# Performance work log

Measured on AMD Instinct MI355X. Metric: run time of the kernel, lower is better.

## Reference

```python
import jax, jax.numpy as jnp
import numpy as np

TAU = 2.0      # LIF membrane time constant (spikingjelly default-style, decay_input=True)
VTH = 0.5      # v_threshold from init
S = 4          # time_steps
EPS = 1e-5     # BatchNorm eps
ALPHA = 4.0    # surrogate sigmoid alpha (spikingjelly Sigmoid default)

@jax.custom_vjp
def spike(x):
    # Heaviside forward (spikingjelly: x >= 0 -> 1)
    return (x >= 0.0).astype(x.dtype)

def _spike_fwd(x):
    return spike(x), x

def _spike_bwd(x, g):
    sg = jax.nn.sigmoid(ALPHA * x)
    return (g * ALPHA * sg * (1.0 - sg),)

spike.defvjp(_spike_fwd, _spike_bwd)

def bn(y, gamma, beta, mean, var):
    # inference-mode BatchNorm2d over channel axis 1; y: (B, C, T, V)
    inv = gamma * jax.lax.rsqrt(var + EPS)
    return y * inv[None, :, None, None] + (beta - mean * inv)[None, :, None, None]


def setup_inputs() -> dict:
    key = jax.random.key(0)
    ks = jax.random.split(key, 16)
    B, T, C, V, H, NC = 16, 512, 3, 16, 128, 12
    inp = {
        "x": jax.random.normal(ks[0], (B, T, C, V), dtype=jnp.float32),
        "w1": jax.random.normal(ks[1], (H, C), dtype=jnp.float32) * (1.0 / np.sqrt(C)),
        "b1": jax.random.normal(ks[2], (H,), dtype=jnp.float32) * 0.01,
        "g1": jnp.ones((H,), jnp.float32),
        "be1": jnp.zeros((H,), jnp.float32),
        "m1": jax.random.normal(ks[3], (H,), dtype=jnp.float32) * 0.1,
        "rv1": jax.random.uniform(ks[4], (H,), dtype=jnp.float32) + 0.5,
        "w2": jax.random.normal(ks[5], (H, H), dtype=jnp.float32) * (1.0 / np.sqrt(H)),
        "b2": jax.random.normal(ks[6], (H,), dtype=jnp.float32) * 0.01,
        "g2": jnp.ones((H,), jnp.float32),
        "be2": jnp.zeros((H,), jnp.float32),
        "m2": jax.random.normal(ks[7], (H,), dtype=jnp.float32) * 0.1,
        "rv2": jax.random.uniform(ks[8], (H,), dtype=jnp.float32) + 0.5,
        "wc": jax.random.normal(ks[9], (NC, H), dtype=jnp.float32) * (1.0 / np.sqrt(H)),
        "bc": jax.random.normal(ks[10], (NC,), dtype=jnp.float32) * 0.01,
    }
    return inp


def reference(x, w1, b1, g1, be1, m1, rv1, w2, b2, g2, be2, m2, rv2, wc, bc):
    # x: (B, T, C, V) -> channels-first (B, C, T, V) as in torch permute
    xc = jnp.transpose(x, (0, 2, 1, 3))
    # fc1 1x1 conv + BN; input identical across all S steps, so compute once
    h1 = bn(jnp.einsum('bctv,oc->botv', xc, w1) + b1[None, :, None, None],
            g1, be1, m1, rv1)  # (B, H, T, V)

    def step(carry, _):
        v1s, v2s, acc = carry
        # LIF1: decay_input=True, v_reset=0 hard reset
        v1n = v1s + (h1 - v1s) / TAU
        s1 = spike(v1n - VTH)
        v1n = v1n * (1.0 - s1)
        # fc2 1x1 conv + BN on spikes
        h2 = bn(jnp.einsum('botv,po->bptv', s1, w2) + b2[None, :, None, None],
                g2, be2, m2, rv2)
        # LIF2
        v2n = v2s + (h2 - v2s) / TAU
        s2 = spike(v2n - VTH)
        v2n = v2n * (1.0 - s2)
        return (v1n, v2n, acc + s2), None

    z = jnp.zeros_like(h1)
    (_, _, acc), _ = jax.lax.scan(step, (z, z, z), None, length=S)
    # mean over S, then mean over T and V -> (B, H); dropout is identity in eval
    feat = (acc / S).mean(axis=(2, 3))
    return feat @ wc.T + bc
```

## Files before the change

### kernel.cpp

```cpp
#include <hip/hip_runtime.h>
#include <hip/hip_bf16.h>
#include <stdint.h>
#include <math.h>

#define B_ 16
#define T_ 512
#define V_ 16
#define H_ 128
#define NC_ 12

typedef float v2f __attribute__((ext_vector_type(2)));
typedef __attribute__((ext_vector_type(8))) short s8frag;
typedef __attribute__((ext_vector_type(16))) float f16frag;
typedef unsigned long long u64;


__device__ __forceinline__ unsigned short bf16_rne(float w) {
    unsigned u = __float_as_uint(w);
    unsigned r = (u + 0x7FFFu + ((u >> 16) & 1u)) >> 16;
    return (unsigned short)r;
}
__device__ __forceinline__ float bf16_f32(unsigned short h) {
    return __uint_as_float((unsigned)h << 16);
}
__device__ __forceinline__ void split8(const float* __restrict__ s, s8frag& hi, s8frag& lo) {
    #pragma unroll
    for (int j = 0; j < 8; ++j) {
        float w = s[j];
        unsigned short hb = bf16_rne(w);
        unsigned short lb = bf16_rne(w - bf16_f32(hb));
        hi[j] = (short)hb;
        lo[j] = (short)lb;
    }
}
__device__ __forceinline__ uint4 expand8(unsigned bt) {
    uint4 r;
    r.x = ((bt      & 1u) * 0x3F80u) | (((bt >> 1) & 1u) * 0x3F800000u);
    r.y = (((bt >> 2) & 1u) * 0x3F80u) | (((bt >> 3) & 1u) * 0x3F800000u);
    r.z = (((bt >> 4) & 1u) * 0x3F80u) | (((bt >> 5) & 1u) * 0x3F800000u);
    r.w = (((bt >> 6) & 1u) * 0x3F80u) | (((bt >> 7) & 1u) * 0x3F800000u);
    return r;
}

#define ROUNDS 8
__global__ __launch_bounds__(256, 3) void snn_main(
    const float* __restrict__ x,
    const float* __restrict__ w1, const float* __restrict__ b1,
    const float* __restrict__ g1, const float* __restrict__ be1,
    const float* __restrict__ m1, const float* __restrict__ rv1,
    const float* __restrict__ w2, const float* __restrict__ b2,
    const float* __restrict__ g2, const float* __restrict__ be2,
    const float* __restrict__ m2, const float* __restrict__ rv2,
    float* __restrict__ feat)
{
    __shared__ uint4 afrag[2][2][8][64];
    __shared__ uint4 msk[4][16];

    const int tid  = threadIdx.x;
    const int lane = tid & 63;
    const int wv   = tid >> 6;
    const int nl   = lane & 15;
    const int kg   = (lane >> 4) & 1;
    const int ch4  = lane >> 5;
    const int bb   = blockIdx.x >> 6;
    const int sbase = (blockIdx.x & 63) * (ROUNDS * 16);

    const int p = lane, q = lane + 64;
    v2f w0v = { w1[p*3+0], w1[q*3+0] };
    v2f w1v = { w1[p*3+1], w1[q*3+1] };
    v2f w2v = { w1[p*3+2], w1[q*3+2] };
    v2f b1v = { b1[p], b1[q] };
    float i1a = g1[p] * (float)(1.0 / sqrt((double)(rv1[p] + 1e-5f)));
    float i1b = g1[q] * (float)(1.0 / sqrt((double)(rv1[q] + 1e-5f)));
    v2f i1v = { i1a, i1b };
    v2f d1v = { be1[p] - m1[p] * i1a, be1[q] - m1[q] * i1b };

    const int chn = wv * 32 + (lane & 31);
    float i2c = g2[chn] * (float)(1.0 / sqrt((double)(rv2[chn] + 1e-5f)));
    float d2c = be2[chn] - m2[chn] * i2c;
    float b2c = b2[chn];

    s8frag bh[8], bl[8];
    #pragma unroll
    for (int c = 0; c < 8; ++c)
        split8(&w2[chn * H_ + c * 16 + ch4 * 8], bh[c], bl[c]);

    float facc = 0.f;

    #define CONSUME(BUF)                                                        \
        for (int tt = 0; tt < 2; ++tt) {                                        \
            f16frag acch = {0.f,0.f,0.f,0.f,0.f,0.f,0.f,0.f,                    \
                            0.f,0.f,0.f,0.f,0.f,0.f,0.f,0.f};                   \
            f16frag accl = acch;                                                \
            _Pragma("unroll")                                                   \
            for (int c = 0; c < 8; ++c) {                                       \
                s8frag a = *(const s8frag*)&afrag[BUF][tt][c][lane];            \
                acch = __builtin_amdgcn_mfma_f32_32x32x16_bf16(a, bh[c], acch, 0,0,0); \
                accl = __builtin_amdgcn_mfma_f32_32x32x16_bf16(a, bl[c], accl, 0,0,0); \
            }                                                                   \
            f16frag accs = acch + accl;                                         \
            _Pragma("unroll")                                                   \
            for (int g = 0; g < 4; ++g) {                                       \
                float v = 0.f;                                                  \
                _Pragma("unroll")                                               \
                for (int s = 0; s < 4; ++s) {                                   \
                    float h2 = (accs[g*4+s] + b2c) * i2c + d2c;                 \
                    v = v + (h2 - v) * 0.5f;                                    \
                    bool sp = v >= 0.5f;                                        \
                    v = sp ? 0.f : v;                                           \
                    facc += sp ? 1.f : 0.f;                                     \
                }                                                               \
            }                                                                   \
        }

    for (int r = 0; r < ROUNDS; ++r) {
        #pragma unroll
        for (int i = 0; i < 4; ++i) {
            int site = sbase + r * 16 + wv * 4 + i;
            int t = site >> 4, v = site & 15;
            const float* xp = x + ((size_t)(bb * T_ + t) * 3) * V_ + v;
            float x0 = xp[0], x1 = xp[V_], x2 = xp[2 * V_];

            v2f h1 = ((x0 * w0v + x1 * w1v + x2 * w2v) + b1v) * i1v + d1v;
            v2f v1t = h1 * 0.5f;
            v2f v2t = v1t + h1 * 0.25f;
            v2f v3t = v2t + (h1 - v2t) * 0.5f;
            v2f v4t = v3t + (h1 - v3t) * 0.5f;

            u64 t1a = __ballot(v1t.x >= 0.5f), t2a = __ballot(v2t.x >= 0.5f);
            u64 t3a = __ballot(v3t.x >= 0.5f), t4a = __ballot(v4t.x >= 0.5f);
            u64 t1b = __ballot(v1t.y >= 0.5f), t2b = __ballot(v2t.y >= 0.5f);
            u64 t3b = __ballot(v3t.y >= 0.5f), t4b = __ballot(v4t.y >= 0.5f);
            u64 s3a = t1a | (t3a & ~t2a), s3b = t1b | (t3b & ~t2b);
            u64 s4a = t2a | (t4a & ~t3a), s4b = t2b | (t4b & ~t3b);

            u64 mx = (lane == 0) ? t1a : (lane == 1) ? t2a : (lane == 2) ? s3a : s4a;
            u64 my = (lane == 0) ? t1b : (lane == 1) ? t2b : (lane == 2) ? s3b : s4b;
            if (lane < 4) {
                uint4 mm;
                mm.x = (unsigned)mx; mm.y = (unsigned)(mx >> 32);
                mm.z = (unsigned)my; mm.w = (unsigned)(my >> 32);
                msk[wv][i * 4 + lane] = mm;
            }
        }
        {
            uint4 mm = msk[wv][nl];
            u64 wsel = ch4 ? ((u64)mm.z | ((u64)mm.w << 32))
                           : ((u64)mm.x | ((u64)mm.y << 32));
            int tt   = wv >> 1;
            int slot = ((wv & 1) * 16 + nl) + 32 * kg;
            int buf  = r & 1;
            #pragma unroll
            for (int j = 0; j < 4; ++j) {
                unsigned by = (unsigned)(wsel >> (kg * 8 + j * 16)) & 0xFFu;
                afrag[buf][tt][ch4 * 4 + j][slot] = expand8(by);
            }
        }
        if (r > 0) { int pb = (r - 1) & 1; CONSUME(pb); }
        __syncthreads();
    }
    { int pb = (ROUNDS - 1) & 1; CONSUME(pb); }
    #undef CONSUME

    facc += __shfl_xor(facc, 32);
    if (lane < 32) atomicAdd(&feat[bb * H_ + chn], facc);
}

__global__ __launch_bounds__(128) void classifier_kernel(
    const float* __restrict__ feat,
    const float* __restrict__ wc,
    const float* __restrict__ bc,
    float* __restrict__ out) {
    __shared__ float fb[H_];
    int b = blockIdx.x, t = threadIdx.x;
    fb[t] = feat[b * H_ + t] * (1.0f / 32768.0f);
    __syncthreads();
    if (t < NC_) {
        float s = 0.f;
        for (int h = 0; h < H_; ++h) s += fb[h] * wc[t * H_ + h];
        out[b * NC_ + t] = s + bc[t];
    }
}

extern "C" void kernel_launch(void* const* d_in, const int* in_sizes, int n_in,
                              void* d_out, int out_size, void* d_ws, size_t ws_size,
                              hipStream_t stream) {
    const float* x   = (const float*)d_in[0];
    const float* w1  = (const float*)d_in[1];
    const float* b1  = (const float*)d_in[2];
    const float* g1  = (const float*)d_in[3];
    const float* be1 = (const float*)d_in[4];
    const float* m1  = (const float*)d_in[5];
    const float* rv1 = (const float*)d_in[6];
    const float* w2  = (const float*)d_in[7];
    const float* b2  = (const float*)d_in[8];
    const float* g2  = (const float*)d_in[9];
    const float* be2 = (const float*)d_in[10];
    const float* m2  = (const float*)d_in[11];
    const float* rv2 = (const float*)d_in[12];
    const float* wc  = (const float*)d_in[13];
    const float* bc  = (const float*)d_in[14];

    float* feat = (float*)d_ws;
    float* out  = (float*)d_out;

    snn_main<<<1024, 256, 0, stream>>>(x, w1, b1, g1, be1, m1, rv1,
                                       w2, b2, g2, be2, m2, rv2, feat);
    classifier_kernel<<<B_, 128, 0, stream>>>(feat, wc, bc, out);
}
```

Before: 141.5 us.

## Fuse classifier into main kernel, fold BN into weights, expand spikes in registers

Several changes land together. The BN2 scale is folded into the split bf16 weights and the bias is folded into the accumulator init. Spike masks are stored as u64 words in shared memory and expanded to bf16 fragments in registers inside the MFMA loop, replacing the pre-expanded afrag buffer. The grid doubles to 2048 blocks of 4 rounds with launch bounds relaxed, and a last-block-done atomic counter computes the classifier in the same kernel, removing the second launch. The done counter is never reset between calls and feat is still not zeroed in the kernel, so the code relies on the harness clearing the workspace; otherwise repeated calls break the last-block test.

```diff
diff --git a/kernel.cpp b/kernel.cpp
--- a/kernel.cpp
+++ b/kernel.cpp
@@ -23,10 +23,11 @@
 __device__ __forceinline__ float bf16_f32(unsigned short h) {
     return __uint_as_float((unsigned)h << 16);
 }
-__device__ __forceinline__ void split8(const float* __restrict__ s, s8frag& hi, s8frag& lo) {
+__device__ __forceinline__ void split8s(const float* __restrict__ s, float scale,
+                                        s8frag& hi, s8frag& lo) {
     #pragma unroll
     for (int j = 0; j < 8; ++j) {
-        float w = s[j];
+        float w = s[j] * scale;
         unsigned short hb = bf16_rne(w);
         unsigned short lb = bf16_rne(w - bf16_f32(hb));
         hi[j] = (short)hb;
@@ -42,8 +43,8 @@
     return r;
 }
 
-#define ROUNDS 8
-__global__ __launch_bounds__(256, 3) void snn_main(
+#define ROUNDS 4
+__global__ __launch_bounds__(256) void snn_main(
     const float* __restrict__ x,
     const float* __restrict__ w1, const float* __restrict__ b1,
     const float* __restrict__ g1, const float* __restrict__ be1,
@@ -51,19 +52,24 @@
     const float* __restrict__ w2, const float* __restrict__ b2,
     const float* __restrict__ g2, const float* __restrict__ be2,
     const float* __restrict__ m2, const float* __restrict__ rv2,
-    float* __restrict__ feat)
+    const float* __restrict__ wc, const float* __restrict__ bc,
+    float* __restrict__ feat, float* __restrict__ done,
+    float* __restrict__ out)
 {
-    __shared__ uint4 afrag[2][2][8][64];
-    __shared__ uint4 msk[4][16];
+    __shared__ union {
+        u64   msk[2][128];
+        float fb[B_ * H_];
+    } sh;
+    __shared__ float lastf;
 
     const int tid  = threadIdx.x;
     const int lane = tid & 63;
     const int wv   = tid >> 6;
-    const int nl   = lane & 15;
-    const int kg   = (lane >> 4) & 1;
-    const int ch4  = lane >> 5;
-    const int bb   = blockIdx.x >> 6;
-    const int sbase = (blockIdx.x & 63) * (ROUNDS * 16);
+    const int hl5  = lane >> 5;
+    const int si   = (lane & 31) >> 2;
+    const int st   = lane & 3;
+    const int bb   = blockIdx.x >> 7;
+    const int sbase = (blockIdx.x & 127) * (ROUNDS * 16);
 
     const int p = lane, q = lane + 64;
     v2f w0v = { w1[p*3+0], w1[q*3+0] };
@@ -78,23 +84,31 @@
     const int chn = wv * 32 + (lane & 31);
     float i2c = g2[chn] * (float)(1.0 / sqrt((double)(rv2[chn] + 1e-5f)));
     float d2c = be2[chn] - m2[chn] * i2c;
-    float b2c = b2[chn];
+    float e2  = b2[chn] * i2c + d2c;
 
     s8frag bh[8], bl[8];
     #pragma unroll
     for (int c = 0; c < 8; ++c)
-        split8(&w2[chn * H_ + c * 16 + ch4 * 8], bh[c], bl[c]);
+        split8s(&w2[chn * H_ + c * 16 + hl5 * 8], i2c, bh[c], bl[c]);
 
     float facc = 0.f;
 
-    #define CONSUME(BUF)                                                        \
+    #define CONSUME(PB)                                                         \
+        _Pragma("unroll")                                                       \
         for (int tt = 0; tt < 2; ++tt) {                                        \
-            f16frag acch = {0.f,0.f,0.f,0.f,0.f,0.f,0.f,0.f,                    \
-                            0.f,0.f,0.f,0.f,0.f,0.f,0.f,0.f};                   \
-            f16frag accl = acch;                                                \
+            u64 mm0 = sh.msk[PB][(tt * 8 + si) * 8 + st * 2 + 0];               \
+            u64 mm1 = sh.msk[PB][(tt * 8 + si) * 8 + st * 2 + 1];               \
+            f16frag acch = { e2,e2,e2,e2,e2,e2,e2,e2,                           \
+                             e2,e2,e2,e2,e2,e2,e2,e2 };                         \
+            f16frag accl = { 0.f,0.f,0.f,0.f,0.f,0.f,0.f,0.f,                   \
+                             0.f,0.f,0.f,0.f,0.f,0.f,0.f,0.f };                 \
             _Pragma("unroll")                                                   \
             for (int c = 0; c < 8; ++c) {                                       \
-                s8frag a = *(const s8frag*)&afrag[BUF][tt][c][lane];            \
+                u64 src = (c < 4) ? mm0 : mm1;                                  \
+                unsigned by = (unsigned)(src >> (((c & 3) * 2 + hl5) * 8)) & 0xFFu; \
+                uint4 fr = expand8(by);                                         \
+                s8frag a;                                                       \
+                ((uint4*)&a)[0] = fr;                                           \
                 acch = __builtin_amdgcn_mfma_f32_32x32x16_bf16(a, bh[c], acch, 0,0,0); \
                 accl = __builtin_amdgcn_mfma_f32_32x32x16_bf16(a, bl[c], accl, 0,0,0); \
             }                                                                   \
@@ -104,7 +118,7 @@
                 float v = 0.f;                                                  \
                 _Pragma("unroll")                                               \
                 for (int s = 0; s < 4; ++s) {                                   \
-                    float h2 = (accs[g*4+s] + b2c) * i2c + d2c;                 \
+                    float h2 = accs[g * 4 + s];                                 \
                     v = v + (h2 - v) * 0.5f;                                    \
                     bool sp = v >= 0.5f;                                        \
                     v = sp ? 0.f : v;                                           \
@@ -116,7 +130,8 @@
     for (int r = 0; r < ROUNDS; ++r) {
         #pragma unroll
         for (int i = 0; i < 4; ++i) {
-            int site = sbase + r * 16 + wv * 4 + i;
+            int sl   = wv * 4 + i;
+            int site = sbase + r * 16 + sl;
             int t = site >> 4, v = site & 15;
             const float* xp = x + ((size_t)(bb * T_ + t) * 3) * V_ + v;
             float x0 = xp[0], x1 = xp[V_], x2 = xp[2 * V_];
@@ -134,51 +149,35 @@
             u64 s3a = t1a | (t3a & ~t2a), s3b = t1b | (t3b & ~t2b);
             u64 s4a = t2a | (t4a & ~t3a), s4b = t2b | (t4b & ~t3b);
 
-            u64 mx = (lane == 0) ? t1a : (lane == 1) ? t2a : (lane == 2) ? s3a : s4a;
-            u64 my = (lane == 0) ? t1b : (lane == 1) ? t2b : (lane == 2) ? s3b : s4b;
-            if (lane < 4) {
-                uint4 mm;
-                mm.x = (unsigned)mx; mm.y = (unsigned)(mx >> 32);
-                mm.z = (unsigned)my; mm.w = (unsigned)(my >> 32);
-                msk[wv][i * 4 + lane] = mm;
+            u64 mA = (lane == 0) ? t1a : (lane == 2) ? t2a : (lane == 4) ? s3a : s4a;
+            u64 mB = (lane == 1) ? t1b : (lane == 3) ? t2b : (lane == 5) ? s3b : s4b;
+            if (lane < 8) {
+                sh.msk[r & 1][sl * 8 + lane] = (lane & 1) ? mB : mA;
             }
         }
-        {
-            uint4 mm = msk[wv][nl];
-            u64 wsel = ch4 ? ((u64)mm.z | ((u64)mm.w << 32))
-                           : ((u64)mm.x | ((u64)mm.y << 32));
-            int tt   = wv >> 1;
-            int slot = ((wv & 1) * 16 + nl) + 32 * kg;
-            int buf  = r & 1;
-            #pragma unroll
-            for (int j = 0; j < 4; ++j) {
-                unsigned by = (unsigned)(wsel >> (kg * 8 + j * 16)) & 0xFFu;
-                afrag[buf][tt][ch4 * 4 + j][slot] = expand8(by);
-            }
-        }
-        if (r > 0) { int pb = (r - 1) & 1; CONSUME(pb); }
+        if (r > 0) { CONSUME((r - 1) & 1) }
         __syncthreads();
     }
-    { int pb = (ROUNDS - 1) & 1; CONSUME(pb); }
+    CONSUME((ROUNDS - 1) & 1)
     #undef CONSUME
 
     facc += __shfl_xor(facc, 32);
     if (lane < 32) atomicAdd(&feat[bb * H_ + chn], facc);
-}
-
-__global__ __launch_bounds__(128) void classifier_kernel(
-    const float* __restrict__ feat,
-    const float* __restrict__ wc,
-    const float* __restrict__ bc,
-    float* __restrict__ out) {
-    __shared__ float fb[H_];
-    int b = blockIdx.x, t = threadIdx.x;
-    fb[t] = feat[b * H_ + t] * (1.0f / 32768.0f);
+
     __syncthreads();
-    if (t < NC_) {
-        float s = 0.f;
-        for (int h = 0; h < H_; ++h) s += fb[h] * wc[t * H_ + h];
-        out[b * NC_ + t] = s + bc[t];
+    if (tid == 0) lastf = atomicAdd(done, 1.0f);
+    __syncthreads();
+    if (lastf >= 2046.5f) {
+        for (int i = tid; i < B_ * H_; i += 256)
+            sh.fb[i] = atomicAdd(&feat[i], 0.0f) * (1.0f / 32768.0f);
+        __syncthreads();
+        if (tid < B_ * NC_) {
+            int b = tid / NC_, n = tid % NC_;
+            float s = 0.f;
+            #pragma unroll 8
+            for (int h = 0; h < H_; ++h) s += sh.fb[b * H_ + h] * wc[n * H_ + h];
+            out[tid] = s + bc[n];
+        }
     }
 }
 
@@ -201,10 +200,12 @@
     const float* wc  = (const float*)d_in[13];
     const float* bc  = (const float*)d_in[14];
 
-    float* feat = (float*)d_ws;
+    float* ws   = (float*)d_ws;
+    float* feat = ws;
+    float* done = ws + B_ * H_;
     float* out  = (float*)d_out;
 
-    snn_main<<<1024, 256, 0, stream>>>(x, w1, b1, g1, be1, m1, rv1,
-                                       w2, b2, g2, be2, m2, rv2, feat);
-    classifier_kernel<<<B_, 128, 0, stream>>>(feat, wc, bc, out);
-}
+    snn_main<<<2048, 256, 0, stream>>>(x, w1, b1, g1, be1, m1, rv1,
+                                       w2, b2, g2, be2, m2, rv2,
+                                       wc, bc, feat, done, out);
+}
```

Result: slower. 171.1 us (+21.0%).
